# Kernel optimization log

Measured on AMD Instinct MI355X. Metric: run time of the kernel, lower is better.

The kernel has to match this reference:

```python
import jax, jax.numpy as jnp
import numpy as np

MAX_DIFF = 0.5


def setup_inputs() -> dict:
    key = jax.random.key(0)
    actions = jax.random.normal(key, (4096, 256, 64), dtype=jnp.float32)
    return {"actions": actions}


def reference(actions):
    # actions: [B, T, A]
    # diffs along time, clamped, then reconstruct via prefix sum from actions[:, 0]
    diffs = jnp.clip(jnp.diff(actions, axis=1), -MAX_DIFF, MAX_DIFF)  # [B, T-1, A]
    rest = actions[:, :1, :] + jnp.cumsum(diffs, axis=1)              # [B, T-1, A]
    return jnp.concatenate([actions[:, :1, :], rest], axis=1)         # [B, T, A]
```

## Files before the change

kernel.cpp:

```cpp
#include <hip/hip_runtime.h>
#include <hip/hip_bf16.h>


typedef float v4f __attribute__((ext_vector_type(4)));

__device__ __forceinline__ float clip05(float d) {
    return fminf(fmaxf(d, -0.5f), 0.5f);
}

__device__ __forceinline__ v4f clipdiff(v4f a, v4f b) {
    v4f r;
    r.x = clip05(a.x - b.x);
    r.y = clip05(a.y - b.y);
    r.z = clip05(a.z - b.z);
    r.w = clip05(a.w - b.w);
    return r;
}

__global__ __launch_bounds__(256) void smooth_scan(
    const float* __restrict__ in, float* __restrict__ out) {
    constexpr int T  = 256;
    constexpr int A4 = 16;
    constexpr int NV = T * A4;

    __shared__ v4f tile[NV];
    __shared__ v4f tot[16][A4];
    __shared__ v4f offt[16][A4];

    const int tid = threadIdx.x;
    const size_t base = (size_t)blockIdx.x * NV;
    const v4f* __restrict__ ip = (const v4f*)in + base;
    v4f*       __restrict__ op = (v4f*)out + base;

#pragma unroll
    for (int k = 0; k < 16; ++k)
        tile[tid + 256 * k] = __builtin_nontemporal_load(ip + tid + 256 * k);
    __syncthreads();

    const int a4  = tid & 15;
    const int seg = tid >> 4;
    const v4f first = tile[a4];
    v4f prev = (seg == 0) ? first : tile[(seg * 16 - 1) * A4 + a4];
    __syncthreads();

    v4f run = (v4f){0.f, 0.f, 0.f, 0.f};
#pragma unroll
    for (int i = 0; i < 16; ++i) {
        const int idx = (seg * 16 + i) * A4 + a4;
        const v4f cur = tile[idx];
        run += clipdiff(cur, prev);
        prev = cur;
        tile[idx] = run;
    }
    tot[seg][a4] = run;
    __syncthreads();

    v4f off = first;
    for (int s = 0; s < seg; ++s) off += tot[s][a4];
    offt[seg][a4] = off;
    __syncthreads();

#pragma unroll
    for (int k = 0; k < 16; ++k) {
        const int f = tid + 256 * k;
        __builtin_nontemporal_store(tile[f] + offt[k][tid & 15], op + f);
    }
}

extern "C" void kernel_launch(void* const* d_in, const int* in_sizes, int n_in,
                              void* d_out, int out_size, void* d_ws, size_t ws_size,
                              hipStream_t stream) {
    const float* in = (const float*)d_in[0];
    float* out = (float*)d_out;

    constexpr int B = 4096;
    smooth_scan<<<B, 256, 0, stream>>>(in, out);
}
```

Baseline: 419.5 us.

## Double-buffer time chunks in LDS with async global-to-LDS loads

```diff
diff --git a/kernel.cpp b/kernel.cpp
--- a/kernel.cpp
+++ b/kernel.cpp
@@ -1,5 +1,4 @@
 #include <hip/hip_runtime.h>
-#include <hip/hip_bf16.h>
 
 
 typedef float v4f __attribute__((ext_vector_type(4)));
@@ -17,53 +16,94 @@
     return r;
 }
 
-__global__ __launch_bounds__(256) void smooth_scan(
+__device__ __forceinline__ void ldst16(const v4f* g, v4f* l) {
+    __builtin_amdgcn_global_load_lds(
+        (const __attribute__((address_space(1))) void*)g,
+        (__attribute__((address_space(3))) void*)l,
+        16, 0, 0);
+}
+
+__global__ __launch_bounds__(256, 4) void smooth_scan(
     const float* __restrict__ in, float* __restrict__ out) {
-    constexpr int T  = 256;
-    constexpr int A4 = 16;
-    constexpr int NV = T * A4;
+    constexpr int A4  = 16;
+    constexpr int CV  = 64 * A4;
+    constexpr int NCH = 4;
 
-    __shared__ v4f tile[NV];
+    __shared__ v4f buf[2][CV];
     __shared__ v4f tot[16][A4];
-    __shared__ v4f offt[16][A4];
+    __shared__ v4f carry[2][A4];
+    __shared__ v4f rawprev[A4];
 
     const int tid = threadIdx.x;
-    const size_t base = (size_t)blockIdx.x * NV;
+    const int a4  = tid & 15;
+    const int seg = tid >> 4;
+    const size_t base = (size_t)blockIdx.x * (NCH * CV);
     const v4f* __restrict__ ip = (const v4f*)in + base;
     v4f*       __restrict__ op = (v4f*)out + base;
 
 #pragma unroll
-    for (int k = 0; k < 16; ++k)
-        tile[tid + 256 * k] = __builtin_nontemporal_load(ip + tid + 256 * k);
-    __syncthreads();
-
-    const int a4  = tid & 15;
-    const int seg = tid >> 4;
-    const v4f first = tile[a4];
-    v4f prev = (seg == 0) ? first : tile[(seg * 16 - 1) * A4 + a4];
-    __syncthreads();
-
-    v4f run = (v4f){0.f, 0.f, 0.f, 0.f};
-#pragma unroll
-    for (int i = 0; i < 16; ++i) {
-        const int idx = (seg * 16 + i) * A4 + a4;
-        const v4f cur = tile[idx];
-        run += clipdiff(cur, prev);
-        prev = cur;
-        tile[idx] = run;
-    }
-    tot[seg][a4] = run;
-    __syncthreads();
-
-    v4f off = first;
-    for (int s = 0; s < seg; ++s) off += tot[s][a4];
-    offt[seg][a4] = off;
-    __syncthreads();
+    for (int j = 0; j < 4; ++j)
+        ldst16(ip + tid + 256 * j, &buf[0][tid + 256 * j]);
+    asm volatile("s_waitcnt vmcnt(0)" ::: "memory");
+    __builtin_amdgcn_s_barrier();
 
 #pragma unroll
-    for (int k = 0; k < 16; ++k) {
-        const int f = tid + 256 * k;
-        __builtin_nontemporal_store(tile[f] + offt[k][tid & 15], op + f);
+    for (int c = 0; c < NCH; ++c) {
+        v4f* bp = buf[c & 1];
+
+        if (c > 0) {
+            asm volatile("s_waitcnt vmcnt(4)" ::: "memory");
+            __builtin_amdgcn_s_barrier();
+        }
+
+        const v4f first = bp[a4];
+        v4f prev = (seg == 0) ? ((c == 0) ? first : rawprev[a4])
+                              : bp[(seg * 4 - 1) * A4 + a4];
+        v4f runs[4];
+        v4f run = (v4f){0.f, 0.f, 0.f, 0.f};
+        v4f cur = prev;
+#pragma unroll
+        for (int i = 0; i < 4; ++i) {
+            cur = bp[(seg * 4 + i) * A4 + a4];
+            run += clipdiff(cur, prev);
+            prev = cur;
+            runs[i] = run;
+        }
+        tot[seg][a4] = run;
+
+        asm volatile("s_waitcnt lgkmcnt(0)" ::: "memory");
+        __builtin_amdgcn_s_barrier();
+
+        if (c + 1 < NCH) {
+            v4f* nb = buf[(c + 1) & 1];
+            const v4f* np = ip + (c + 1) * CV;
+#pragma unroll
+            for (int j = 0; j < 4; ++j)
+                ldst16(np + tid + 256 * j, &nb[tid + 256 * j]);
+        }
+
+        v4f off = (c == 0) ? first : carry[c & 1][a4];
+#pragma unroll
+        for (int s = 0; s < 15; ++s) {
+            const v4f tv = tot[s][a4];
+            if (s < seg) off += tv;
+        }
+#pragma unroll
+        for (int i = 0; i < 4; ++i)
+            bp[(seg * 4 + i) * A4 + a4] = off + runs[i];
+        if (seg == 15) {
+            carry[(c + 1) & 1][a4] = off + runs[3];
+            rawprev[a4] = cur;
+        }
+
+        asm volatile("s_waitcnt lgkmcnt(0)" ::: "memory");
+        __builtin_amdgcn_s_barrier();
+
+#pragma unroll
+        for (int j = 0; j < 4; ++j) {
+            const int f = tid + 256 * j;
+            __builtin_nontemporal_store(bp[f], op + c * CV + f);
+        }
     }
 }
 
```

Measured after the change: 449.4 us. 1.07x slower.

## Replace LDS tile scan with per-wavefront streaming shuffle scan

Applied to the files above, without the earlier changes.

```diff
diff --git a/kernel.cpp b/kernel.cpp
--- a/kernel.cpp
+++ b/kernel.cpp
@@ -1,5 +1,4 @@
 #include <hip/hip_runtime.h>
-#include <hip/hip_bf16.h>
 
 
 typedef float v4f __attribute__((ext_vector_type(4)));
@@ -17,53 +16,73 @@
     return r;
 }
 
+__device__ __forceinline__ v4f shflv(v4f x, int srcLane) {
+    v4f r;
+    r.x = __shfl(x.x, srcLane, 64);
+    r.y = __shfl(x.y, srcLane, 64);
+    r.z = __shfl(x.z, srcLane, 64);
+    r.w = __shfl(x.w, srcLane, 64);
+    return r;
+}
+
+__device__ __forceinline__ v4f shflupv(v4f x, int delta) {
+    v4f r;
+    r.x = __shfl_up(x.x, delta, 64);
+    r.y = __shfl_up(x.y, delta, 64);
+    r.z = __shfl_up(x.z, delta, 64);
+    r.w = __shfl_up(x.w, delta, 64);
+    return r;
+}
+
 __global__ __launch_bounds__(256) void smooth_scan(
     const float* __restrict__ in, float* __restrict__ out) {
-    constexpr int T  = 256;
     constexpr int A4 = 16;
-    constexpr int NV = T * A4;
+    constexpr int NV = 256 * A4;
 
-    __shared__ v4f tile[NV];
-    __shared__ v4f tot[16][A4];
-    __shared__ v4f offt[16][A4];
+    const int tid  = threadIdx.x;
+    const int lane = tid & 63;
+    const int tsub = lane >> 4;
+    const int a4   = lane & 15;
+    const int b    = blockIdx.x * 4 + (tid >> 6);
 
-    const int tid = threadIdx.x;
-    const size_t base = (size_t)blockIdx.x * NV;
-    const v4f* __restrict__ ip = (const v4f*)in + base;
-    v4f*       __restrict__ op = (v4f*)out + base;
+    const v4f* __restrict__ ip = (const v4f*)in + (size_t)b * NV;
+    v4f*       __restrict__ op = (v4f*)out + (size_t)b * NV;
 
-#pragma unroll
-    for (int k = 0; k < 16; ++k)
-        tile[tid + 256 * k] = __builtin_nontemporal_load(ip + tid + 256 * k);
-    __syncthreads();
+    v4f v  = __builtin_nontemporal_load(ip + lane);
+    v4f pv = __builtin_nontemporal_load(ip + 64 + lane);
 
-    const int a4  = tid & 15;
-    const int seg = tid >> 4;
-    const v4f first = tile[a4];
-    v4f prev = (seg == 0) ? first : tile[(seg * 16 - 1) * A4 + a4];
-    __syncthreads();
+    v4f xp = shflupv(v, 16);
+    v4f cd = (tsub == 0) ? (v4f){0.f, 0.f, 0.f, 0.f} : clipdiff(v, xp);
+    v4f s = shflupv(cd, 16);
+    if (tsub >= 1) cd += s;
+    s = shflupv(cd, 32);
+    if (tsub >= 2) cd += s;
 
-    v4f run = (v4f){0.f, 0.f, 0.f, 0.f};
-#pragma unroll
-    for (int i = 0; i < 16; ++i) {
-        const int idx = (seg * 16 + i) * A4 + a4;
-        const v4f cur = tile[idx];
-        run += clipdiff(cur, prev);
-        prev = cur;
-        tile[idx] = run;
-    }
-    tot[seg][a4] = run;
-    __syncthreads();
+    v4f carry = shflv(v, a4);
+    v4f o = carry + cd;
+    __builtin_nontemporal_store(o, op + lane);
+    carry     = shflv(o, 48 + a4);
+    v4f xlast = shflv(v, 48 + a4);
+    v = pv;
 
-    v4f off = first;
-    for (int s = 0; s < seg; ++s) off += tot[s][a4];
-    offt[seg][a4] = off;
-    __syncthreads();
+    for (int t0 = 4; t0 < 256; t0 += 4) {
+        v4f nv;
+        if (t0 + 4 < 256)
+            nv = __builtin_nontemporal_load(ip + (t0 + 4) * A4 + lane);
 
-#pragma unroll
-    for (int k = 0; k < 16; ++k) {
-        const int f = tid + 256 * k;
-        __builtin_nontemporal_store(tile[f] + offt[k][tid & 15], op + f);
+        xp = shflupv(v, 16);
+        if (tsub == 0) xp = xlast;
+        cd = clipdiff(v, xp);
+        s = shflupv(cd, 16);
+        if (tsub >= 1) cd += s;
+        s = shflupv(cd, 32);
+        if (tsub >= 2) cd += s;
+
+        o = carry + cd;
+        __builtin_nontemporal_store(o, op + t0 * A4 + lane);
+        carry = shflv(o, 48 + a4);
+        xlast = shflv(v, 48 + a4);
+        v = nv;
     }
 }
 
@@ -73,6 +92,5 @@
     const float* in = (const float*)d_in[0];
     float* out = (float*)d_out;
 
-    constexpr int B = 4096;
-    smooth_scan<<<B, 256, 0, stream>>>(in, out);
+    smooth_scan<<<1024, 256, 0, stream>>>(in, out);
 }
```

Measured after the change: 441.7 us. 1.05x slower.
